# Kernel optimization log

Measured on AMD Instinct MI355X. Metric: run time of the kernel, lower is better.

## Reference

```python
import jax, jax.numpy as jnp
import numpy as np

GRID_SIZE = 3
SPLINE_ORDER = 3
GRID_RANGE = (-1.0, 1.0)


def make_grid():
    # extended knot vector, shape (1, grid_size + 2*spline_order + 1) = (1, 10)
    h = (GRID_RANGE[1] - GRID_RANGE[0]) / GRID_SIZE
    pts = np.arange(-SPLINE_ORDER, GRID_SIZE + SPLINE_ORDER + 1, dtype=np.float32) * h + GRID_RANGE[0]
    return jnp.asarray(pts[None, :])  # broadcasts over in_features


def b_splines(x, grid):
    # x: (B, in) -> bases: (B, in, grid_size + spline_order)
    x = x[..., None]  # (B, in, 1)
    bases = ((x >= grid[:, :-1]) & (x < grid[:, 1:])).astype(x.dtype)
    for k in range(1, SPLINE_ORDER + 1):
        left = (x - grid[:, : -(k + 1)]) / (grid[:, k:-1] - grid[:, : -(k + 1)])
        right = (grid[:, k + 1:] - x) / (grid[:, k + 1:] - grid[:, 1:-k])
        bases = left * bases[..., :-1] + right * bases[..., 1:]
    return bases


def kan_linear(x, base_w, spline_w, scaler, grid):
    # efficient-kan KANLinear: silu(x)@base_w.T + b_splines(x) contracted with scaled spline weights
    base_out = jnp.einsum('bi,oi->bo', jax.nn.silu(x), base_w)
    bases = b_splines(x, grid)  # (B, in, 6)
    spline_out = jnp.einsum('bik,oik->bo', bases, spline_w * scaler[..., None])
    return base_out + spline_out


def layer_norm(x, gamma, beta, eps=1e-5):
    mu = jnp.mean(x, axis=-1, keepdims=True)
    var = jnp.mean(jnp.square(x - mu), axis=-1, keepdims=True)
    return (x - mu) * jax.lax.rsqrt(var + eps) * gamma + beta


def setup_inputs() -> dict:
    key = jax.random.key(0)
    ks = jax.random.split(key, 8)
    B, D_IN, D_HID, D_OUT = 16384, 1280, 512, 229
    NB = GRID_SIZE + SPLINE_ORDER  # 6 basis functions per input feature
    s1 = 1.0 / np.sqrt(D_IN)
    s2 = 1.0 / np.sqrt(D_HID)
    return {
        'x': jax.random.normal(ks[0], (B, D_IN), dtype=jnp.float32),
        'base_w1': jax.random.normal(ks[1], (D_HID, D_IN), dtype=jnp.float32) * s1,
        'spline_w1': jax.random.normal(ks[2], (D_HID, D_IN, NB), dtype=jnp.float32) * s1,
        'scaler1': jax.random.normal(ks[3], (D_HID, D_IN), dtype=jnp.float32) * 0.1 + 1.0,
        'ln_gamma': jnp.ones((D_HID,), dtype=jnp.float32),
        'ln_beta': jnp.zeros((D_HID,), dtype=jnp.float32),
        'base_w2': jax.random.normal(ks[4], (D_OUT, D_HID), dtype=jnp.float32) * s2,
        'spline_w2': jax.random.normal(ks[5], (D_OUT, D_HID, NB), dtype=jnp.float32) * s2,
        'scaler2': jax.random.normal(ks[6], (D_OUT, D_HID), dtype=jnp.float32) * 0.1 + 1.0,
    }


def reference(x, base_w1, spline_w1, scaler1, ln_gamma, ln_beta, base_w2, spline_w2, scaler2):
    grid = make_grid()
    h = kan_linear(x, base_w1, spline_w1, scaler1, grid)   # (B, 512)
    h = layer_norm(h, ln_gamma, ln_beta)                    # dropout: identity at inference
    out = kan_linear(h, base_w2, spline_w2, scaler2, grid)  # (B, 229)
    return out
```

## Files before the change

kernel.cpp:

```cpp
#include <hip/hip_runtime.h>


typedef short s16x8 __attribute__((ext_vector_type(8)));
typedef float f32x4 __attribute__((ext_vector_type(4)));
typedef float f32x16 __attribute__((ext_vector_type(16)));

__device__ __forceinline__ unsigned pk2(float lo, float hi) {
  unsigned a = __float_as_uint(lo), b = __float_as_uint(hi);
  a = a + 0x7fffu + ((a >> 16) & 1u);
  b = b + 0x7fffu + ((b >> 16) & 1u);
  return __builtin_amdgcn_perm(b, a, 0x07060302u);
}

__device__ __forceinline__ unsigned short f2bf(float f) {
  unsigned u = __float_as_uint(f);
  unsigned r = u + 0x7fffu + ((u >> 16) & 1u);
  return (unsigned short)(r >> 16);
}

__device__ __forceinline__ s16x8 kan_act8(float x) {
  float e = __expf(-x);
  float s = x * __builtin_amdgcn_rcpf(1.0f + e);
  float u = fmaf(x, 1.5f, 4.5f);
  float d[10];
#pragma unroll
  for (int j = 0; j < 10; ++j) d[j] = u - (float)j;
  float b1[8];
#pragma unroll
  for (int j = 0; j < 8; ++j) b1[j] = fmaxf(0.0f, 1.0f - fabsf(d[j + 1]));
  float B2[7];
#pragma unroll
  for (int j = 0; j < 7; ++j) B2[j] = d[j] * b1[j] - d[j + 3] * b1[j + 1];
  float b3[6];
#pragma unroll
  for (int j = 0; j < 6; ++j)
    b3[j] = d[j] * B2[j] - d[j + 4] * B2[j + 1];
  union { uint4 u4; s16x8 v; } r;
  r.u4.x = pk2(s, b3[0]);
  r.u4.y = pk2(b3[1], b3[2]);
  r.u4.z = pk2(b3[3], b3[4]);
  r.u4.w = pk2(b3[5], 0.0f);
  return r.v;
}

__global__ __launch_bounds__(256) void prep_w(
    const float* __restrict__ base_w, const float* __restrict__ spline_w,
    const float* __restrict__ scaler, short* __restrict__ WT,
    int F, int Ncols, int Nvalid) {
  int i = blockIdx.x * 256 + threadIdx.x;
  int n = blockIdx.y;
  if (i >= F) return;
  s16x8 v;
#pragma unroll
  for (int k = 0; k < 8; ++k) v[k] = 0;
  if (n < Nvalid) {
    int idx = n * F + i;
    float sc = scaler[idx] * (1.0f / 6.0f);
    v[0] = (short)f2bf(base_w[idx]);
#pragma unroll
    for (int k = 0; k < 6; ++k) v[1 + k] = (short)f2bf(spline_w[idx * 6 + k] * sc);
  }
  *(s16x8*)&WT[((size_t)i * Ncols + n) * 8] = v;
}

template <int NT>
__global__ __launch_bounds__(512, 2) void kan_gemm(
    const float* __restrict__ X, const short* __restrict__ WT,
    float* __restrict__ Cp, int F, int span, long long pstride, int ldc) {
  constexpr int Ncols = NT * 256;
  __shared__ __align__(16) short As[2][64 * 64];

  const int t  = threadIdx.x;
  const int lane = t & 63;
  const int w  = t >> 6;
  const int r5 = lane & 31;
  const int hi = lane >> 5;
  const int m0 = blockIdx.x * 64;
  const int f0 = blockIdx.z * span;
  const int c0 = w * (NT * 32);
  const int s3 = r5 & 7;
  const int a_lo = r5 * 64;

  const int sr = t >> 3, sj = t & 7;
  const float* xq = X + (size_t)(m0 + sr) * F + f0 + sj;
  const int aw = sr * 64 + ((sj ^ (sr & 7)) * 8);

  const s16x8* wpt = (const s16x8*)WT + (size_t)(f0 + hi) * Ncols + c0 + r5;

  f32x16 acc[2][NT] = {};
  const int nss = span >> 3;

  s16x8 bc[4][NT], bn[4][NT];
#pragma unroll
  for (int kq = 0; kq < 4; ++kq)
#pragma unroll
    for (int nt = 0; nt < NT; ++nt)
      bc[kq][nt] = wpt[(size_t)(kq * 2) * Ncols + nt * 32];
  {
    s16x8 a = kan_act8(xq[0]);
    *(s16x8*)&As[0][aw] = a;
  }
  float xn1 = xq[8];
  float xn2 = xq[16 < span ? 16 : 8];
  __syncthreads();

  for (int ss = 0; ss < nss; ++ss) {
    const int cb = ss & 1, nb = cb ^ 1;
    const bool more = (ss + 1 < nss);

    int pf = ss + 3 < nss ? ss + 3 : nss - 1;
    float xn0 = xq[(size_t)pf * 8];

    if (more) {
      const s16x8* wn = wpt + (size_t)(ss + 1) * 8 * Ncols;
#pragma unroll
      for (int kq = 0; kq < 4; ++kq)
#pragma unroll
        for (int nt = 0; nt < NT; ++nt)
          bn[kq][nt] = wn[(size_t)(kq * 2) * Ncols + nt * 32];
    }

    const short* Ac = As[cb];
#pragma unroll
    for (int kq = 0; kq < 4; ++kq) {
      const int co = ((kq * 2 + hi) ^ s3) * 8;
      s16x8 a0 = *(const s16x8*)(Ac + a_lo + co);
      s16x8 a1 = *(const s16x8*)(Ac + a_lo + 2048 + co);
#pragma unroll
      for (int nt = 0; nt < NT; ++nt) {
        acc[0][nt] = __builtin_amdgcn_mfma_f32_32x32x16_bf16(
            a0, bc[kq][nt], acc[0][nt], 0, 0, 0);
        acc[1][nt] = __builtin_amdgcn_mfma_f32_32x32x16_bf16(
            a1, bc[kq][nt], acc[1][nt], 0, 0, 0);
      }
    }

    if (more) {
      s16x8 a = kan_act8(xn1);
      *(s16x8*)&As[nb][aw] = a;
      xn1 = xn2; xn2 = xn0;
    }
    asm volatile("s_waitcnt lgkmcnt(0)" ::: "memory");
    __builtin_amdgcn_s_barrier();
#pragma unroll
    for (int kq = 0; kq < 4; ++kq)
#pragma unroll
      for (int nt = 0; nt < NT; ++nt)
        bc[kq][nt] = bn[kq][nt];
  }

  float* cpt = Cp + (size_t)blockIdx.z * (size_t)pstride;
#pragma unroll
  for (int mt = 0; mt < 2; ++mt) {
#pragma unroll
    for (int nt = 0; nt < NT; ++nt) {
      int col = c0 + nt * 32 + r5;
#pragma unroll
      for (int reg = 0; reg < 16; ++reg) {
        int row = m0 + mt * 32 + (reg & 3) + 8 * (reg >> 2) + 4 * hi;
        cpt[(size_t)row * ldc + col] = acc[mt][nt][reg];
      }
    }
  }
}

__global__ __launch_bounds__(256) void ln_reduce(
    const float* __restrict__ p0, const float* __restrict__ p1,
    float* __restrict__ h, const float* __restrict__ gamma,
    const float* __restrict__ beta, int nparts) {
  int lane = threadIdx.x & 63;
  int wv   = threadIdx.x >> 6;
  int row  = blockIdx.x * 4 + wv;
  size_t base = (size_t)row * 512 + lane * 8;
  f32x4 v0 = *(const f32x4*)(p0 + base);
  f32x4 v1 = *(const f32x4*)(p0 + base + 4);
  if (nparts == 2) {
    f32x4 u0 = *(const f32x4*)(p1 + base);
    f32x4 u1 = *(const f32x4*)(p1 + base + 4);
#pragma unroll
    for (int k = 0; k < 4; ++k) { v0[k] += u0[k]; v1[k] += u1[k]; }
  }
  float s = 0.f, s2 = 0.f;
#pragma unroll
  for (int k = 0; k < 4; ++k) { s += v0[k] + v1[k]; s2 += v0[k]*v0[k] + v1[k]*v1[k]; }
#pragma unroll
  for (int m = 32; m >= 1; m >>= 1) {
    s  += __shfl_xor(s,  m, 64);
    s2 += __shfl_xor(s2, m, 64);
  }
  float mean = s * (1.0f / 512.0f);
  float var  = s2 * (1.0f / 512.0f) - mean * mean;
  float rstd = rsqrtf(var + 1e-5f);
  const f32x4 g0 = *(const f32x4*)(gamma + lane * 8);
  const f32x4 g1 = *(const f32x4*)(gamma + lane * 8 + 4);
  const f32x4 be0 = *(const f32x4*)(beta + lane * 8);
  const f32x4 be1 = *(const f32x4*)(beta + lane * 8 + 4);
#pragma unroll
  for (int k = 0; k < 4; ++k) {
    v0[k] = (v0[k] - mean) * rstd * g0[k] + be0[k];
    v1[k] = (v1[k] - mean) * rstd * g1[k] + be1[k];
  }
  *(f32x4*)(h + base) = v0;
  *(f32x4*)(h + base + 4) = v1;
}

__global__ __launch_bounds__(256) void out_reduce(
    const float* __restrict__ p0, const float* __restrict__ p1,
    float* __restrict__ out, int nparts) {
  int idx = blockIdx.x * 256 + threadIdx.x;
  int row = idx >> 8;
  int c   = idx & 255;
  float v = p0[idx];
  if (nparts == 2) v += p1[idx];
  if (c < 229) out[(size_t)row * 229 + c] = v;
}

extern "C" void kernel_launch(void* const* d_in, const int* in_sizes, int n_in,
                              void* d_out, int out_size, void* d_ws, size_t ws_size,
                              hipStream_t stream) {
  const float* x         = (const float*)d_in[0];
  const float* base_w1   = (const float*)d_in[1];
  const float* spline_w1 = (const float*)d_in[2];
  const float* scaler1   = (const float*)d_in[3];
  const float* ln_gamma  = (const float*)d_in[4];
  const float* ln_beta   = (const float*)d_in[5];
  const float* base_w2   = (const float*)d_in[6];
  const float* spline_w2 = (const float*)d_in[7];
  const float* scaler2   = (const float*)d_in[8];
  float* out = (float*)d_out;

  const int B = 16384, D_IN = 1280, D_HID = 512, D_OUT = 229;

  const size_t szW1 = (size_t)D_IN * D_HID * 8 * 2;
  const size_t szW2 = (size_t)D_HID * 256 * 8 * 2;
  const size_t szH  = (size_t)B * D_HID * 4;
  const size_t szP  = (size_t)B * 512 * 4;
  char* ws = (char*)d_ws;
  short* W1p = (short*)ws;
  short* W2p = (short*)(ws + szW1);
  float* h   = (float*)(ws + szW1 + szW2);
  float* p0  = (float*)(ws + szW1 + szW2 + szH);
  float* p1  = (float*)(ws + szW1 + szW2 + szH + szP);

  const int parts = (ws_size >= szW1 + szW2 + szH + 2 * szP) ? 2 : 1;
  const long long pstride = (long long)(szP / 4);

  prep_w<<<dim3(D_IN / 256, D_HID), 256, 0, stream>>>(
      base_w1, spline_w1, scaler1, W1p, D_IN, D_HID, D_HID);
  prep_w<<<dim3(D_HID / 256, 256), 256, 0, stream>>>(
      base_w2, spline_w2, scaler2, W2p, D_HID, 256, D_OUT);

  kan_gemm<2><<<dim3(B / 64, 1, parts), 512, 0, stream>>>(
      x, W1p, p0, D_IN, D_IN / parts, pstride, D_HID);

  ln_reduce<<<dim3(B / 4), 256, 0, stream>>>(p0, p1, h, ln_gamma, ln_beta, parts);

  kan_gemm<1><<<dim3(B / 64, 1, parts), 512, 0, stream>>>(
      h, W2p, p0, D_HID, D_HID / parts, pstride, 256);

  out_reduce<<<dim3(B * 256 / 256), 256, 0, stream>>>(p0, p1, out, parts);
}
```

Before: 444.2 us.

## Split GEMM column tiles across blocks with 256-thread blocks

The KAN GEMM now uses 256-thread blocks that each cover 256 output columns, with a grid y-dimension over column tiles, in place of 512-thread blocks covering all columns. Every block uses the same per-wave tile of 64 columns (two 32-column MFMA tiles). Each thread now computes two activation rows per staging step, so each of the two blocks per row tile for the first layer recomputes the B-spline activations. The aim is better occupancy and scheduling, at the cost of duplicated activation work and duplicated X loads in layer 1.

```diff
diff --git a/kernel.cpp b/kernel.cpp
--- a/kernel.cpp
+++ b/kernel.cpp
@@ -63,11 +63,10 @@
   *(s16x8*)&WT[((size_t)i * Ncols + n) * 8] = v;
 }
 
-template <int NT>
-__global__ __launch_bounds__(512, 2) void kan_gemm(
+template <int Ncols>
+__global__ __launch_bounds__(256, 3) void kan_gemm(
     const float* __restrict__ X, const short* __restrict__ WT,
     float* __restrict__ Cp, int F, int span, long long pstride, int ldc) {
-  constexpr int Ncols = NT * 256;
   __shared__ __align__(16) short As[2][64 * 64];
 
   const int t  = threadIdx.x;
@@ -76,32 +75,37 @@
   const int r5 = lane & 31;
   const int hi = lane >> 5;
   const int m0 = blockIdx.x * 64;
+  const int bc0 = blockIdx.y * 256;
   const int f0 = blockIdx.z * span;
-  const int c0 = w * (NT * 32);
+  const int c0 = bc0 + w * 64;
   const int s3 = r5 & 7;
   const int a_lo = r5 * 64;
 
-  const int sr = t >> 3, sj = t & 7;
+  const int sr = t >> 2, sj = t & 3;
   const float* xq = X + (size_t)(m0 + sr) * F + f0 + sj;
-  const int aw = sr * 64 + ((sj ^ (sr & 7)) * 8);
+  const int aw0 = sr * 64 + ((sj ^ (sr & 7)) * 8);
+  const int aw1 = sr * 64 + (((sj + 4) ^ (sr & 7)) * 8);
 
   const s16x8* wpt = (const s16x8*)WT + (size_t)(f0 + hi) * Ncols + c0 + r5;
 
-  f32x16 acc[2][NT] = {};
+  f32x16 acc[2][2] = {};
   const int nss = span >> 3;
 
-  s16x8 bc[4][NT], bn[4][NT];
+  s16x8 bc[4][2], bn[4][2];
 #pragma unroll
   for (int kq = 0; kq < 4; ++kq)
 #pragma unroll
-    for (int nt = 0; nt < NT; ++nt)
+    for (int nt = 0; nt < 2; ++nt)
       bc[kq][nt] = wpt[(size_t)(kq * 2) * Ncols + nt * 32];
   {
-    s16x8 a = kan_act8(xq[0]);
-    *(s16x8*)&As[0][aw] = a;
-  }
-  float xn1 = xq[8];
-  float xn2 = xq[16 < span ? 16 : 8];
+    s16x8 a0 = kan_act8(xq[0]);
+    *(s16x8*)&As[0][aw0] = a0;
+    s16x8 a1 = kan_act8(xq[4]);
+    *(s16x8*)&As[0][aw1] = a1;
+  }
+  float xA0 = xq[8],  xA1 = xq[12];
+  float xB0 = xq[16 < span ? 16 : 8];
+  float xB1 = xq[16 < span ? 20 : 12];
   __syncthreads();
 
   for (int ss = 0; ss < nss; ++ss) {
@@ -110,13 +114,14 @@
 
     int pf = ss + 3 < nss ? ss + 3 : nss - 1;
     float xn0 = xq[(size_t)pf * 8];
+    float xn1 = xq[(size_t)pf * 8 + 4];
 
     if (more) {
       const s16x8* wn = wpt + (size_t)(ss + 1) * 8 * Ncols;
 #pragma unroll
       for (int kq = 0; kq < 4; ++kq)
 #pragma unroll
-        for (int nt = 0; nt < NT; ++nt)
+        for (int nt = 0; nt < 2; ++nt)
           bn[kq][nt] = wn[(size_t)(kq * 2) * Ncols + nt * 32];
     }
 
@@ -127,7 +132,7 @@
       s16x8 a0 = *(const s16x8*)(Ac + a_lo + co);
       s16x8 a1 = *(const s16x8*)(Ac + a_lo + 2048 + co);
 #pragma unroll
-      for (int nt = 0; nt < NT; ++nt) {
+      for (int nt = 0; nt < 2; ++nt) {
         acc[0][nt] = __builtin_amdgcn_mfma_f32_32x32x16_bf16(
             a0, bc[kq][nt], acc[0][nt], 0, 0, 0);
         acc[1][nt] = __builtin_amdgcn_mfma_f32_32x32x16_bf16(
@@ -136,16 +141,18 @@
     }
 
     if (more) {
-      s16x8 a = kan_act8(xn1);
-      *(s16x8*)&As[nb][aw] = a;
-      xn1 = xn2; xn2 = xn0;
+      s16x8 a0 = kan_act8(xA0);
+      *(s16x8*)&As[nb][aw0] = a0;
+      s16x8 a1 = kan_act8(xA1);
+      *(s16x8*)&As[nb][aw1] = a1;
+      xA0 = xB0; xA1 = xB1; xB0 = xn0; xB1 = xn1;
     }
     asm volatile("s_waitcnt lgkmcnt(0)" ::: "memory");
     __builtin_amdgcn_s_barrier();
 #pragma unroll
     for (int kq = 0; kq < 4; ++kq)
 #pragma unroll
-      for (int nt = 0; nt < NT; ++nt)
+      for (int nt = 0; nt < 2; ++nt)
         bc[kq][nt] = bn[kq][nt];
   }
 
@@ -153,7 +160,7 @@
 #pragma unroll
   for (int mt = 0; mt < 2; ++mt) {
 #pragma unroll
-    for (int nt = 0; nt < NT; ++nt) {
+    for (int nt = 0; nt < 2; ++nt) {
       int col = c0 + nt * 32 + r5;
 #pragma unroll
       for (int reg = 0; reg < 16; ++reg) {
@@ -250,12 +257,12 @@
   prep_w<<<dim3(D_HID / 256, 256), 256, 0, stream>>>(
       base_w2, spline_w2, scaler2, W2p, D_HID, 256, D_OUT);
 
-  kan_gemm<2><<<dim3(B / 64, 1, parts), 512, 0, stream>>>(
+  kan_gemm<512><<<dim3(B / 64, 2, parts), 256, 0, stream>>>(
       x, W1p, p0, D_IN, D_IN / parts, pstride, D_HID);
 
   ln_reduce<<<dim3(B / 4), 256, 0, stream>>>(p0, p1, h, ln_gamma, ln_beta, parts);
 
-  kan_gemm<1><<<dim3(B / 64, 1, parts), 512, 0, stream>>>(
+  kan_gemm<256><<<dim3(B / 64, 1, parts), 256, 0, stream>>>(
       h, W2p, p0, D_HID, D_HID / parts, pstride, 256);
 
   out_reduce<<<dim3(B * 256 / 256), 256, 0, stream>>>(p0, p1, out, parts);
```

New measurement: 459.3 us. 3.4% more time.
